# Optimization experiments

Measured on AMD Instinct MI355X. Metric: run time of the kernel, lower is better.

Reference implementation:

```python
import jax, jax.numpy as jnp
import numpy as np

R = 4          # args.search_range
D = 2 * R + 1  # window size per axis -> D*D = 81 output channels


def setup_inputs() -> dict:
    key = jax.random.key(0)
    k1, k2 = jax.random.split(key)
    B, C, H, W = 4, 128, 64, 128
    src = jax.random.normal(k1, (B, C, H, W), dtype=jnp.float32)
    tgt = jax.random.normal(k2, (B, C, H, W), dtype=jnp.float32)
    return {"src": src, "tgt": tgt}


def reference(src, tgt):
    # Faithful to the torch code: tgt is zero-padded by R on each spatial side,
    # then for output pixel (i, j) the window indices into the PADDED tensor are
    # I in [i-R, i+R], J in [j-R, j+R]. For i < R the index is negative, which in
    # torch wraps around -> reproduce with modular indexing.
    B, C, H, W = src.shape
    tp = jnp.pad(tgt, ((0, 0), (0, 0), (R, R), (R, R)))  # [B,C,H+2R,W+2R]
    Hp, Wp = H + 2 * R, W + 2 * R
    # col_idx[dj, j] = (j - R + dj) mod Wp
    col_idx = (jnp.arange(W)[None, :] - R + jnp.arange(D)[:, None]) % Wp  # [D,W]
    outs = []
    for di in range(D):  # small fixed loop over 9 row offsets
        row_idx = (jnp.arange(H) - R + di) % Hp        # [H]
        t_rows = tp[:, :, row_idx, :]                  # [B,C,H,Wp]
        t_win = t_rows[:, :, :, col_idx]               # [B,C,H,D,W]
        # channel-dot-product per pixel and per column offset
        outs.append(jnp.einsum('bchdw,bchw->bdhw', t_win, src))
    # channel ordering k = di*D + dj matches the original double loop over (I, J)
    return jnp.concatenate(outs, axis=1)  # [B, D*D, H, W]
```

## Files before the change

### kernel.cpp

```cpp
#include <hip/hip_runtime.h>
#include <stdint.h>

#define NB 4
#define NC 128
#define NH 64
#define NW 128
#define HW (NH * NW)
#define ND 9
#define NOUT (ND * ND)
#define SH 4
#define QW 32
#define TROW 392
#define SROW 264
#define OTILE (ND * 32)

typedef __attribute__((ext_vector_type(8))) short short8;
typedef __attribute__((ext_vector_type(4))) float f32x4;

__device__ __forceinline__ ushort f2bf(float f) {
  uint u = __float_as_uint(f);
  u += 0x7FFFu + ((u >> 16) & 1u);
  return (ushort)(u >> 16);
}

__global__ __launch_bounds__(576, 1) void costvol_kernel(const float* __restrict__ src,
                                                         const float* __restrict__ tgt,
                                                         float* __restrict__ out) {
  __shared__ ushort tgtS[9][16 * TROW];
  __shared__ ushort srcS[SH][16 * SROW];
  __shared__ float  outlds[ND * OTILE];

  const int tid  = threadIdx.x;
  const int lane = tid & 63;
  const int wave = tid >> 6;
  const int col  = lane & 15;
  const int g    = lane >> 4;

  const int xcd   = blockIdx.x & 7;
  const int r     = blockIdx.x >> 3;
  const int combo = ((r >> 4) << 3) | xcd;
  const int b     = combo >> 2;
  const int q     = combo & 3;
  const int h0    = (r & 15) << 2;

  const float* sb = src + (size_t)(b * NC) * HW;
  const float* tb = tgt + (size_t)(b * NC) * HW;

  auto stage_tgt = [&](int y) {
    ushort* dstS = tgtS[y % 9];
    const float* py = tb + (size_t)y * NW;
    for (int cell = tid; cell < 12 * 128; cell += 576) {
      const int fc = cell % 12;
      const int c  = cell / 12;
      const int g0 = q * QW - 16 + 4 * fc;
      const float4 v = *(const float4*)(py + (size_t)c * HW + (g0 < 0 ? 0 : g0));
      ushort* d = dstS + (c >> 3) * TROW + (4 * fc) * 8 + (c & 7);
      d[0]  = f2bf(v.x);
      d[8]  = f2bf(v.y);
      d[16] = f2bf(v.z);
      d[24] = f2bf(v.w);
    }
  };
  auto stage_src = [&](int hh) {
    ushort* dstS = srcS[hh];
    const float* ph = sb + (size_t)(h0 + hh) * NW + q * QW;
    for (int cell = tid; cell < 8 * 128; cell += 576) {
      const int fc = cell % 8;
      const int c  = cell / 8;
      const float4 v = *(const float4*)(ph + (size_t)c * HW + 4 * fc);
      ushort* d = dstS + (c >> 3) * SROW + (4 * fc) * 8 + (c & 7);
      d[0]  = f2bf(v.x);
      d[8]  = f2bf(v.y);
      d[16] = f2bf(v.z);
      d[24] = f2bf(v.w);
    }
  };

#pragma unroll
  for (int hh = 0; hh < SH; ++hh) stage_src(hh);
  for (int y = h0 - 8; y <= h0; ++y)
    if (y >= 0) stage_tgt(y);
  __syncthreads();

  for (int hh = 0; hh < SH; ++hh) {
    const int h = h0 + hh;
    const int y = h + wave - 8;
    if (y >= 0) {
      const ushort* Bp = tgtS[y % 9];
      const ushort* Ap = srcS[hh];
      f32x4 aD0 = {0.f,0.f,0.f,0.f}, aS0 = {0.f,0.f,0.f,0.f};
      f32x4 aD1 = {0.f,0.f,0.f,0.f}, aS1 = {0.f,0.f,0.f,0.f};
#pragma unroll
      for (int kk = 0; kk < 4; ++kk) {
        const int ro = 4 * kk + g;
        const short8 A0 = *(const short8*)&Ap[ro * SROW + col * 8];
        const short8 A1 = *(const short8*)&Ap[ro * SROW + (16 + col) * 8];
        const short8 B0 = *(const short8*)&Bp[ro * TROW + col * 8];
        const short8 B1 = *(const short8*)&Bp[ro * TROW + (16 + col) * 8];
        const short8 B2 = *(const short8*)&Bp[ro * TROW + (32 + col) * 8];
        aS0 = __builtin_amdgcn_mfma_f32_16x16x32_bf16(A0, B0, aS0, 0, 0, 0);
        aD0 = __builtin_amdgcn_mfma_f32_16x16x32_bf16(A0, B1, aD0, 0, 0, 0);
        aS1 = __builtin_amdgcn_mfma_f32_16x16x32_bf16(A1, B1, aS1, 0, 0, 0);
        aD1 = __builtin_amdgcn_mfma_f32_16x16x32_bf16(A1, B2, aD1, 0, 0, 0);
      }
      float* ol = &outlds[wave * OTILE];
#pragma unroll
      for (int qr = 0; qr < 4; ++qr) {
        const int row = 4 * g + qr;
        const int djd = col - row + 8;
        const int djs = col - row - 8;
        if (djd >= 0 && djd <= 8) {
          ol[djd * 32 + ((row + 4 * djd) & 31)]      = aD0[qr];
          ol[djd * 32 + ((16 + row + 4 * djd) & 31)] = aD1[qr];
        }
        if (djs >= 0 && djs <= 8) {
          ol[djs * 32 + ((row + 4 * djs) & 31)]      = aS0[qr];
          ol[djs * 32 + ((16 + row + 4 * djs) & 31)] = aS1[qr];
        }
      }
    }
    __syncthreads();

    for (int s = tid; s < ND * ND * 8; s += 576) {
      const int di = s / 72;
      const int rr = s % 72;
      const int dj = rr >> 3;
      const int w4 = (rr & 7) << 2;
      f32x4 o = *(const f32x4*)&outlds[di * OTILE + dj * 32 + ((w4 + 4 * dj) & 31)];
      const bool vb = (h + di - 8) >= 0;
      const int wg = q * QW + w4;
#pragma unroll
      for (int i = 0; i < 4; ++i)
        if (!vb || (wg + i + dj < 8)) o[i] = 0.f;
      *(f32x4*)(out + ((size_t)((b * NOUT + di * ND + dj) * NH + h)) * NW + wg) = o;
    }
    if (hh < SH - 1) stage_tgt(h + 1);
    __syncthreads();
  }
}

extern "C" void kernel_launch(void* const* d_in, const int* in_sizes, int n_in,
                              void* d_out, int out_size, void* d_ws, size_t ws_size,
                              hipStream_t stream) {
  const float* src = (const float*)d_in[0];
  const float* tgt = (const float*)d_in[1];
  float* out = (float*)d_out;
  costvol_kernel<<<dim3(256), dim3(576), 0, stream>>>(src, tgt, out);
}
```

Before: 92.99 us.

## Vectorize bf16 staging stores and prefetch next target row before MFMA compute

Each thread now loads 8 channels of a float4 column group and writes packed short8 bf16 vectors to LDS, replacing the scalar 2-byte scattered stores. The next target row is prefetched into registers at the top of each row iteration and converted and stored only after the compute and output phases, so its global load latency overlaps the MFMA work. The initial target staging is also flattened into a single loop over all needed rows. The trade-off is higher register pressure from holding eight float4 values per thread, and only 192 of 576 threads carry the prefetch.

New measurement: 86.08 us. 7.4% less time.

```diff
diff --git a/kernel.cpp b/kernel.cpp
--- a/kernel.cpp
+++ b/kernel.cpp
@@ -46,44 +46,64 @@
   const float* sb = src + (size_t)(b * NC) * HW;
   const float* tb = tgt + (size_t)(b * NC) * HW;
 
-  auto stage_tgt = [&](int y) {
-    ushort* dstS = tgtS[y % 9];
-    const float* py = tb + (size_t)y * NW;
-    for (int cell = tid; cell < 12 * 128; cell += 576) {
-      const int fc = cell % 12;
-      const int c  = cell / 12;
+  for (int cell = tid; cell < SH * 128; cell += 576) {
+    const int hh = cell >> 7;
+    const int cc = cell & 127;
+    const int fc = cc & 7;
+    const int o  = cc >> 3;
+    const float* p = sb + (size_t)(h0 + hh) * NW + q * QW + 4 * fc + (size_t)(o * 8) * HW;
+    float4 v[8];
+#pragma unroll
+    for (int j = 0; j < 8; ++j) v[j] = *(const float4*)(p + (size_t)j * HW);
+    ushort* d = srcS[hh] + o * SROW + (4 * fc) * 8;
+#pragma unroll
+    for (int i = 0; i < 4; ++i) {
+      short8 e;
+#pragma unroll
+      for (int j = 0; j < 8; ++j) e[j] = (short)f2bf(((const float*)&v[j])[i]);
+      *(short8*)&d[i * 8] = e;
+    }
+  }
+  {
+    const int y0  = (h0 >= 8) ? h0 - 8 : 0;
+    const int nts = h0 - y0 + 1;
+    for (int cell = tid; cell < nts * 192; cell += 576) {
+      const int y  = y0 + cell / 192;
+      const int cc = cell % 192;
+      const int fc = cc % 12;
+      const int o  = cc / 12;
       const int g0 = q * QW - 16 + 4 * fc;
-      const float4 v = *(const float4*)(py + (size_t)c * HW + (g0 < 0 ? 0 : g0));
-      ushort* d = dstS + (c >> 3) * TROW + (4 * fc) * 8 + (c & 7);
-      d[0]  = f2bf(v.x);
-      d[8]  = f2bf(v.y);
-      d[16] = f2bf(v.z);
-      d[24] = f2bf(v.w);
+      const float* p = tb + (size_t)y * NW + (g0 < 0 ? 0 : g0) + (size_t)(o * 8) * HW;
+      float4 v[8];
+#pragma unroll
+      for (int j = 0; j < 8; ++j) v[j] = *(const float4*)(p + (size_t)j * HW);
+      ushort* d = tgtS[y % 9] + o * TROW + (4 * fc) * 8;
+#pragma unroll
+      for (int i = 0; i < 4; ++i) {
+        short8 e;
+#pragma unroll
+        for (int j = 0; j < 8; ++j) e[j] = (short)f2bf(((const float*)&v[j])[i]);
+        *(short8*)&d[i * 8] = e;
+      }
     }
-  };
-  auto stage_src = [&](int hh) {
-    ushort* dstS = srcS[hh];
-    const float* ph = sb + (size_t)(h0 + hh) * NW + q * QW;
-    for (int cell = tid; cell < 8 * 128; cell += 576) {
-      const int fc = cell % 8;
-      const int c  = cell / 8;
-      const float4 v = *(const float4*)(ph + (size_t)c * HW + 4 * fc);
-      ushort* d = dstS + (c >> 3) * SROW + (4 * fc) * 8 + (c & 7);
-      d[0]  = f2bf(v.x);
-      d[8]  = f2bf(v.y);
-      d[16] = f2bf(v.z);
-      d[24] = f2bf(v.w);
-    }
-  };
-
-#pragma unroll
-  for (int hh = 0; hh < SH; ++hh) stage_src(hh);
-  for (int y = h0 - 8; y <= h0; ++y)
-    if (y >= 0) stage_tgt(y);
+  }
   __syncthreads();
 
   for (int hh = 0; hh < SH; ++hh) {
     const int h = h0 + hh;
+
+    float4 pv[8];
+    const bool hs = (hh < SH - 1) && (tid < 192);
+    int sfc = 0, so = 0;
+    if (hs) {
+      sfc = tid % 12;
+      so  = tid / 12;
+      const int g0 = q * QW - 16 + 4 * sfc;
+      const float* p = tb + (size_t)(h + 1) * NW + (g0 < 0 ? 0 : g0) + (size_t)(so * 8) * HW;
+#pragma unroll
+      for (int j = 0; j < 8; ++j) pv[j] = *(const float4*)(p + (size_t)j * HW);
+    }
+
     const int y = h + wave - 8;
     if (y >= 0) {
       const ushort* Bp = tgtS[y % 9];
@@ -134,7 +154,17 @@
         if (!vb || (wg + i + dj < 8)) o[i] = 0.f;
       *(f32x4*)(out + ((size_t)((b * NOUT + di * ND + dj) * NH + h)) * NW + wg) = o;
     }
-    if (hh < SH - 1) stage_tgt(h + 1);
+
+    if (hs) {
+      ushort* d = tgtS[(h + 1) % 9] + so * TROW + (4 * sfc) * 8;
+#pragma unroll
+      for (int i = 0; i < 4; ++i) {
+        short8 e;
+#pragma unroll
+        for (int j = 0; j < 8; ++j) e[j] = (short)f2bf(((const float*)&pv[j])[i]);
+        *(short8*)&d[i * 8] = e;
+      }
+    }
     __syncthreads();
   }
 }
```
